# Performance work log

Measured on AMD Instinct MI355X. Metric: run time of the kernel, lower is better.

Reference implementation:

```python
import jax, jax.numpy as jnp
import numpy as np

N, E, T, D, M, G = 131072, 524288, 4, 128, 256, 4096
VOCAB, GH, L, PASSES = 100, 512, 128, 4


def setup_inputs() -> dict:
    key = jax.random.key(0)
    ks = jax.random.split(key, 20)
    node_types = jax.random.randint(ks[0], (N,), 0, VOCAB)
    edge_src = jax.random.randint(ks[1], (E,), 0, N)
    edge_dst = jax.random.randint(ks[2], (E,), 0, N)
    edge_type = jax.random.randint(ks[3], (E,), 0, T)
    inner = jnp.sort(jax.random.randint(ks[4], (G - 1,), 0, N))
    ptr = jnp.concatenate([jnp.zeros((1,), jnp.int64 if inner.dtype == jnp.int64 else jnp.int32),
                           inner, jnp.full((1,), N, inner.dtype)])
    s = 1.0 / np.sqrt(D)
    emb = jax.random.normal(ks[5], (VOCAB, D), jnp.float32)
    W_msg = jax.random.normal(ks[6], (T, M, D), jnp.float32) * s
    b_msg = jax.random.normal(ks[7], (T, M), jnp.float32) * s
    W_ih = jax.random.normal(ks[8], (3 * D, M), jnp.float32) * (1.0 / np.sqrt(M))
    W_hh = jax.random.normal(ks[9], (3 * D, D), jnp.float32) * s
    b_ih = jax.random.normal(ks[10], (3 * D,), jnp.float32) * s
    b_hh = jax.random.normal(ks[11], (3 * D,), jnp.float32) * s
    W_gate = jax.random.normal(ks[12], (1, D), jnp.float32) * s
    b_gate = jax.random.normal(ks[13], (1,), jnp.float32) * s
    W_n2g = jax.random.normal(ks[14], (GH, D), jnp.float32) * s
    b_n2g = jax.random.normal(ks[15], (GH,), jnp.float32) * s
    W_loc = jax.random.normal(ks[16], (L, GH), jnp.float32) * (1.0 / np.sqrt(GH))
    b_loc = jax.random.normal(ks[17], (L,), jnp.float32) * (1.0 / np.sqrt(GH))
    W_lv = jax.random.normal(ks[18], (L, GH), jnp.float32) * (1.0 / np.sqrt(GH))
    b_lv = jax.random.normal(ks[19], (L,), jnp.float32) * (1.0 / np.sqrt(GH))
    return dict(node_types=node_types, edge_src=edge_src, edge_dst=edge_dst,
                edge_type=edge_type, ptr=ptr, emb=emb, W_msg=W_msg, b_msg=b_msg,
                W_ih=W_ih, W_hh=W_hh, b_ih=b_ih, b_hh=b_hh, W_gate=W_gate,
                b_gate=b_gate, W_n2g=W_n2g, b_n2g=b_n2g, W_loc=W_loc, b_loc=b_loc,
                W_lv=W_lv, b_lv=b_lv)


def _ggnn_pass(h, edge_src, edge_dst, edge_type, W_msg, b_msg, W_ih, W_hh, b_ih, b_hh):
    # per-edge-type linear on all nodes: [T, N, M]
    msgs_all = jnp.einsum('nd,tmd->tnm', h, W_msg) + b_msg[:, None, :]
    # gather the message of the edge's type at its source node: [E, M]
    e_msg = msgs_all[edge_type, edge_src]
    # sparse adjacency matmul == scatter-add of source messages into destinations
    agg = jax.ops.segment_sum(e_msg, edge_dst, num_segments=h.shape[0])
    m = jax.nn.relu(agg)
    # torch GRUCell
    gi = m @ W_ih.T + b_ih      # [N, 3D]
    gh = h @ W_hh.T + b_hh      # [N, 3D]
    d = h.shape[1]
    ir, iz, inn = gi[:, :d], gi[:, d:2 * d], gi[:, 2 * d:]
    hr, hz, hn = gh[:, :d], gh[:, d:2 * d], gh[:, 2 * d:]
    r = jax.nn.sigmoid(ir + hr)
    z = jax.nn.sigmoid(iz + hz)
    n = jnp.tanh(inn + r * hn)
    return (1.0 - z) * n + z * h


def reference(node_types, edge_src, edge_dst, edge_type, ptr, emb, W_msg, b_msg,
              W_ih, W_hh, b_ih, b_hh, W_gate, b_gate, W_n2g, b_n2g,
              W_loc, b_loc, W_lv, b_lv):
    h = emb[node_types]  # [N, D]
    for _ in range(PASSES):
        h = _ggnn_pass(h, edge_src, edge_dst, edge_type,
                       W_msg, b_msg, W_ih, W_hh, b_ih, b_hh)
    # gated segment readout (equivalent to per-graph attn @ h slices)
    gate = jax.nn.sigmoid(h @ W_gate.T + b_gate)        # [N, 1]
    hg = h @ W_n2g.T + b_n2g                            # [N, GH]
    seg = jnp.searchsorted(ptr, jnp.arange(h.shape[0]), side='right') - 1
    h_graph = jax.ops.segment_sum(gate * hg, seg, num_segments=ptr.shape[0] - 1)
    z_loc = h_graph @ W_loc.T + b_loc
    z_logvar = h_graph @ W_lv.T + b_lv
    return (z_loc, z_logvar)
```

## Files before the change

kernel.cpp:

```cpp
#include <hip/hip_runtime.h>
#include <cstdint>
#include <cstddef>

#define NN 131072
#define EE 524288
#define GG 4096
#define NPASS 4

typedef __attribute__((ext_vector_type(4))) float f32x4;
typedef __attribute__((ext_vector_type(8))) short bfrag;

__device__ __forceinline__ unsigned short f2bf(float f) {
  union { float f; unsigned u; } v; v.f = f;
  unsigned r = v.u + 0x7fffu + ((v.u >> 16) & 1u);
  return (unsigned short)(r >> 16);
}
__device__ __forceinline__ float bf2f(unsigned short h) {
  union { unsigned u; float f; } v; v.u = ((unsigned)h) << 16;
  return v.f;
}
__device__ __forceinline__ unsigned pack2(float x, float y) {
  return (unsigned)f2bf(x) | ((unsigned)f2bf(y) << 16);
}
__device__ __forceinline__ float sigm(float x) { return 1.f / (1.f + __expf(-x)); }

__device__ __forceinline__ void cp16(unsigned short* l, const unsigned short* g) {
  __builtin_amdgcn_global_load_lds(
      (const __attribute__((address_space(1))) unsigned int*)g,
      (__attribute__((address_space(3))) unsigned int*)l, 16, 0, 0);
}

__global__ void prep_wb(const float* __restrict__ Wmsg, unsigned short* __restrict__ Wb) {
  int idx = blockIdx.x * 256 + threadIdx.x;
  if (idx >= 256 * 512) return;
  int m = idx >> 9, k = idx & 511;
  int t = k >> 7, d = k & 127;
  Wb[idx] = f2bf(Wmsg[((size_t)t * 256 + m) * 128 + d]);
}

__global__ void prep_wgru(const float* __restrict__ Wih, const float* __restrict__ Whh,
                          unsigned short* __restrict__ Wgru) {
  int idx = blockIdx.x * 256 + threadIdx.x;
  if (idx >= 512 * 384) return;
  int j = idx / 384, kk = idx % 384;
  float v;
  if (kk < 256) v = (j < 384) ? Wih[j * 256 + kk] : 0.f;
  else          v = (j < 256) ? Whh[j * 128 + (kk - 256)]
                   : ((j >= 384) ? Whh[(j - 128) * 128 + (kk - 256)] : 0.f);
  int g = (j < 128) ? 0 : (j < 256) ? 1 : (j < 384) ? 2 : 3;
  int d = j & 127;
  Wgru[(size_t)(4 * d + g) * 384 + kk] = f2bf(v);
}

__global__ void prep_bias(const float* __restrict__ bih, const float* __restrict__ bhh,
                          float* __restrict__ biasg) {
  int j = blockIdx.x * 256 + threadIdx.x;
  if (j >= 512) return;
  float v;
  if (j < 256) v = bih[j] + bhh[j];
  else if (j < 384) v = bih[j];
  else v = bhh[j - 128];
  int g = (j < 128) ? 0 : (j < 256) ? 1 : (j < 384) ? 2 : 3;
  int d = j & 127;
  biasg[4 * d + g] = v;
}

__global__ void compose_k(const float* __restrict__ Wloc, const float* __restrict__ Wlv,
                          const float* __restrict__ Wn2g, float* __restrict__ WcT) {
  int b = blockIdx.x;
  int jl = threadIdx.x >> 7, d = threadIdx.x & 127;
  int j = b * 2 + jl;
  const float* wx = (j < 128) ? Wloc + (size_t)j * 512 : Wlv + (size_t)(j - 128) * 512;
  float acc = 0.f;
  for (int k = 0; k < 512; k++) acc += wx[k] * Wn2g[k * 128 + d];
  WcT[d * 256 + j] = acc;
}

__global__ void cvec_k(const float* __restrict__ Wloc, const float* __restrict__ Wlv,
                       const float* __restrict__ bn2g, float* __restrict__ cvec) {
  int j = threadIdx.x;
  const float* wx = (j < 128) ? Wloc + (size_t)j * 512 : Wlv + (size_t)(j - 128) * 512;
  float a = 0.f;
  for (int k = 0; k < 512; k++) a += wx[k] * bn2g[k];
  cvec[j] = a;
}

__global__ void init_h(const int* __restrict__ nt, const float* __restrict__ emb,
                       unsigned short* __restrict__ H) {
  size_t idx = (size_t)blockIdx.x * 256 + threadIdx.x;
  int n = (int)(idx >> 7), d = (int)(idx & 127);
  H[idx] = f2bf(emb[(size_t)nt[n] * 128 + d]);
}

__global__ void cnt4_k(const int* __restrict__ edst, const int* __restrict__ etype,
                       int* __restrict__ cnti) {
  int e = blockIdx.x * 256 + threadIdx.x;
  if (e >= EE) return;
  atomicAdd(&cnti[edst[e] * 4 + etype[e]], 1);
}

__global__ void degsum_k(const int* __restrict__ cnti, int* __restrict__ deg,
                         float* __restrict__ cnt) {
  int n = blockIdx.x * 256 + threadIdx.x;
  if (n >= NN) return;
  int4 c4 = *(const int4*)&cnti[n * 4];
  deg[n] = c4.x + c4.y + c4.z + c4.w;
  float4 f4 = make_float4((float)c4.x, (float)c4.y, (float)c4.z, (float)c4.w);
  *(float4*)&cnt[n * 4] = f4;
}

__global__ __launch_bounds__(1024) void scan_k(const int* __restrict__ deg,
                                               int* __restrict__ rowptr,
                                               int* __restrict__ cursor) {
  __shared__ int part[1024];
  int t = threadIdx.x;
  int base = t * 128;
  int s = 0;
  for (int i = 0; i < 128; i++) s += deg[base + i];
  part[t] = s;
  __syncthreads();
  for (int off = 1; off < 1024; off <<= 1) {
    int v = (t >= off) ? part[t - off] : 0;
    __syncthreads();
    part[t] += v;
    __syncthreads();
  }
  int run = part[t] - s;
  for (int i = 0; i < 128; i++) {
    rowptr[base + i] = run;
    cursor[base + i] = run;
    run += deg[base + i];
  }
  if (t == 1023) rowptr[NN] = run;
}

__global__ void fill_k(const int* __restrict__ esrc, const int* __restrict__ edst,
                       const int* __restrict__ etype, int* __restrict__ cursor,
                       unsigned* __restrict__ epack) {
  int e = blockIdx.x * 256 + threadIdx.x;
  if (e >= EE) return;
  int pos = atomicAdd(&cursor[edst[e]], 1);
  epack[pos] = ((unsigned)etype[e] << 17) | (unsigned)esrc[e];
}

__global__ __launch_bounds__(256) void agg_k(const int* __restrict__ rowptr,
                                             const unsigned* __restrict__ epack,
                                             const unsigned short* __restrict__ H,
                                             unsigned short* __restrict__ s) {
  int n = blockIdx.x * 4 + (threadIdx.x >> 6);
  int lane = threadIdx.x & 63;
  int beg = rowptr[n], end = rowptr[n + 1];
  const unsigned short* hbase = H + lane * 2;
  float a0 = 0.f, a1 = 0.f, b0 = 0.f, b1 = 0.f;
  float c0 = 0.f, c1 = 0.f, d0 = 0.f, d1 = 0.f;
#define ACCUM(P, HV)                                              \
  {                                                               \
    int t_ = (int)((P) >> 17);                                    \
    float v0_ = bf2f((unsigned short)((HV) & 0xffffu));           \
    float v1_ = bf2f((unsigned short)((HV) >> 16));               \
    if (t_ == 0)      { a0 += v0_; a1 += v1_; }                   \
    else if (t_ == 1) { b0 += v0_; b1 += v1_; }                   \
    else if (t_ == 2) { c0 += v0_; c1 += v1_; }                   \
    else              { d0 += v0_; d1 += v1_; }                   \
  }
  for (int base = beg; base < end; base += 64) {
    int cnt = end - base;
    if (cnt > 64) cnt = 64;
    int mye = base + lane;
    unsigned ep = (mye < end) ? epack[mye] : 0u;
    if (cnt > 0) {
      unsigned p = (unsigned)__shfl((int)ep, 0);
      unsigned hv = *(const unsigned*)&hbase[(size_t)(p & 0x1FFFFu) * 128];
      for (int j = 1; j < cnt; j++) {
        unsigned pn = (unsigned)__shfl((int)ep, j);
        unsigned hvn = *(const unsigned*)&hbase[(size_t)(pn & 0x1FFFFu) * 128];
        ACCUM(p, hv);
        p = pn;
        hv = hvn;
      }
      ACCUM(p, hv);
    }
  }
#undef ACCUM
  unsigned short* srow = s + (size_t)n * 512;
  *(unsigned*)&srow[0 * 128 + lane * 2] = pack2(a0, a1);
  *(unsigned*)&srow[1 * 128 + lane * 2] = pack2(b0, b1);
  *(unsigned*)&srow[2 * 128 + lane * 2] = pack2(c0, c1);
  *(unsigned*)&srow[3 * 128 + lane * 2] = pack2(d0, d1);
}

__global__ __launch_bounds__(512, 4) void msgemm_k(
    unsigned short* __restrict__ s, const float* __restrict__ cnt,
    const unsigned short* __restrict__ Wb, const float* __restrict__ bmsg) {
  __shared__ __align__(16) unsigned short As[2][128 * 32];
  __shared__ __align__(16) unsigned short Bs[2][256 * 32];
  int i0 = blockIdx.x * 128;
  int tid = threadIdx.x, lane = tid & 63, w = tid >> 6;
  int wi = w >> 1, wj = w & 1;
  int q = lane >> 4, r = lane & 15;
  int srow = tid >> 2;
  int swcol = ((tid & 3) ^ ((srow >> 1) & 3)) * 8;

  const unsigned short* sP = s + (size_t)(i0 + srow) * 512 + swcol;
  const unsigned short* WbP = Wb + (size_t)srow * 512 + swcol;

  int aoff[2], boff[8];
#pragma unroll
  for (int rt = 0; rt < 2; rt++) {
    int row = wi * 32 + rt * 16 + r;
    aoff[rt] = row * 32 + (q ^ ((row >> 1) & 3)) * 8;
  }
#pragma unroll
  for (int ct = 0; ct < 8; ct++) {
    int row = wj * 128 + ct * 16 + r;
    boff[ct] = row * 32 + (q ^ ((row >> 1) & 3)) * 8;
  }

  f32x4 acc[2][8];
#pragma unroll
  for (int a = 0; a < 2; a++)
#pragma unroll
    for (int b = 0; b < 8; b++) acc[a][b] = f32x4{0.f, 0.f, 0.f, 0.f};

  cp16(&As[0][w * 512], sP);
#pragma unroll
  for (int c = 0; c < 2; c++)
    cp16(&Bs[0][c * 4096 + w * 512], WbP + (size_t)(c * 128) * 512);
  __syncthreads();

  for (int ks = 0; ks < 16; ks++) {
    int b = ks & 1;
    if (ks < 15) {
      int nb = b ^ 1;
      cp16(&As[nb][w * 512], sP + (ks + 1) * 32);
#pragma unroll
      for (int c = 0; c < 2; c++)
        cp16(&Bs[nb][c * 4096 + w * 512],
             WbP + (size_t)(c * 128) * 512 + (ks + 1) * 32);
    }
    bfrag af[2];
#pragma unroll
    for (int rt = 0; rt < 2; rt++) af[rt] = *(const bfrag*)&As[b][aoff[rt]];
#pragma unroll
    for (int ct = 0; ct < 8; ct++) {
      bfrag bfr = *(const bfrag*)&Bs[b][boff[ct]];
#pragma unroll
      for (int rt = 0; rt < 2; rt++)
        acc[rt][ct] =
            __builtin_amdgcn_mfma_f32_16x16x32_bf16(af[rt], bfr, acc[rt][ct], 0, 0, 0);
    }
    __syncthreads();
  }

#pragma unroll
  for (int ct = 0; ct < 8; ct++) {
    int j = wj * 128 + ct * 16 + r;
    float b0 = bmsg[j], b1 = bmsg[256 + j], b2 = bmsg[512 + j], b3 = bmsg[768 + j];
#pragma unroll
    for (int rt = 0; rt < 2; rt++) {
#pragma unroll
      for (int reg = 0; reg < 4; reg++) {
        int il = wi * 32 + rt * 16 + q * 4 + reg;
        float4 c4 = *(const float4*)&cnt[(size_t)(i0 + il) * 4];
        float v = acc[rt][ct][reg] + c4.x * b0 + c4.y * b1 + c4.z * b2 + c4.w * b3;
        v = v > 0.f ? v : 0.f;
        s[(size_t)(i0 + il) * 512 + j] = f2bf(v);
      }
    }
  }
}

__global__ __launch_bounds__(512, 4) void grugemm_k(
    const unsigned short* __restrict__ m,
    const unsigned short* __restrict__ Hc, unsigned short* __restrict__ Hn,
    const unsigned short* __restrict__ Wgru, const float* __restrict__ biasg) {
  __shared__ __align__(16) unsigned short As[2][128 * 32];
  __shared__ __align__(16) unsigned short Bs[2][256 * 32];
  int wg = (blockIdx.x & 7) * 256 + (blockIdx.x >> 3);
  int bcol = wg & 1;
  int i0 = (wg >> 1) * 128;
  int tid = threadIdx.x, lane = tid & 63, w = tid >> 6;
  int wi = w >> 1, wj = w & 1;
  int q = lane >> 4, r = lane & 15;
  int srow = tid >> 2;
  int swcol = ((tid & 3) ^ ((srow >> 1) & 3)) * 8;

  const unsigned short* mP = m + (size_t)(i0 + srow) * 512 + swcol;
  const unsigned short* hP = Hc + (size_t)(i0 + srow) * 128 + swcol;
  const unsigned short* WgP = Wgru + (size_t)(bcol * 256 + srow) * 384 + swcol;

  int aoff[2], boff[8];
#pragma unroll
  for (int rt = 0; rt < 2; rt++) {
    int row = wi * 32 + rt * 16 + r;
    aoff[rt] = row * 32 + (q ^ ((row >> 1) & 3)) * 8;
  }
#pragma unroll
  for (int ct = 0; ct < 8; ct++) {
    int row = wj * 128 + ct * 16 + r;
    boff[ct] = row * 32 + (q ^ ((row >> 1) & 3)) * 8;
  }

  f32x4 acc[2][8];
#pragma unroll
  for (int a = 0; a < 2; a++)
#pragma unroll
    for (int b = 0; b < 8; b++) acc[a][b] = f32x4{0.f, 0.f, 0.f, 0.f};

  cp16(&As[0][w * 512], mP);
#pragma unroll
  for (int c = 0; c < 2; c++)
    cp16(&Bs[0][c * 4096 + w * 512], WgP + (size_t)(c * 128) * 384);
  __syncthreads();

  for (int ks = 0; ks < 12; ks++) {
    int b = ks & 1;
    if (ks < 11) {
      int nb = b ^ 1;
      int nks = ks + 1;
      const unsigned short* aSrc =
          (nks < 8) ? (mP + nks * 32) : (hP + (nks - 8) * 32);
      cp16(&As[nb][w * 512], aSrc);
#pragma unroll
      for (int c = 0; c < 2; c++)
        cp16(&Bs[nb][c * 4096 + w * 512],
             WgP + (size_t)(c * 128) * 384 + nks * 32);
    }
    bfrag af[2];
#pragma unroll
    for (int rt = 0; rt < 2; rt++) af[rt] = *(const bfrag*)&As[b][aoff[rt]];
#pragma unroll
    for (int ct = 0; ct < 8; ct++) {
      bfrag bfr = *(const bfrag*)&Bs[b][boff[ct]];
#pragma unroll
      for (int rt = 0; rt < 2; rt++)
        acc[rt][ct] =
            __builtin_amdgcn_mfma_f32_16x16x32_bf16(af[rt], bfr, acc[rt][ct], 0, 0, 0);
    }
    __syncthreads();
  }

  int rr = r & 3;
  bool s1 = (lane & 1) != 0, s2 = (lane & 2) != 0;
#pragma unroll
  for (int ct = 0; ct < 8; ct++) {
    float bias = biasg[bcol * 256 + wj * 128 + ct * 16 + r];
    int d = bcol * 64 + wj * 32 + ct * 4 + (r >> 2);
#pragma unroll
    for (int rt = 0; rt < 2; rt++) {
      float v0 = acc[rt][ct][0] + bias;
      float v1 = acc[rt][ct][1] + bias;
      float v2 = acc[rt][ct][2] + bias;
      float v3 = acc[rt][ct][3] + bias;
      float t, rcv;
      t = s1 ? v0 : v1; rcv = __shfl_xor(t, 1);
      v0 = s1 ? rcv : v0; v1 = s1 ? v1 : rcv;
      t = s1 ? v2 : v3; rcv = __shfl_xor(t, 1);
      v2 = s1 ? rcv : v2; v3 = s1 ? v3 : rcv;
      t = s2 ? v0 : v2; rcv = __shfl_xor(t, 2);
      v0 = s2 ? rcv : v0; v2 = s2 ? v2 : rcv;
      t = s2 ? v1 : v3; rcv = __shfl_xor(t, 2);
      v1 = s2 ? rcv : v1; v3 = s2 ? v3 : rcv;
      int i = i0 + wi * 32 + rt * 16 + q * 4 + rr;
      size_t hoff = (size_t)i * 128 + d;
      float hold = bf2f(Hc[hoff]);
      float rg = sigm(v0), zg = sigm(v1);
      float ng = tanhf(v2 + rg * v3);
      Hn[hoff] = f2bf((1.f - zg) * ng + zg * hold);
    }
  }
}

__global__ __launch_bounds__(256) void gate_k(const unsigned short* __restrict__ H,
                                              const float* __restrict__ Wg,
                                              const float* __restrict__ bg,
                                              float* __restrict__ gate) {
  __shared__ float wg[128];
  if (threadIdx.x < 128) wg[threadIdx.x] = Wg[threadIdx.x];
  __syncthreads();
  int g = threadIdx.x >> 4, sub = threadIdx.x & 15;
  int n = blockIdx.x * 16 + g;
  const unsigned short* hr = H + (size_t)n * 128;
  float p = 0.f;
  for (int k = sub; k < 128; k += 16) p += bf2f(hr[k]) * wg[k];
  p += __shfl_xor(p, 1);
  p += __shfl_xor(p, 2);
  p += __shfl_xor(p, 4);
  p += __shfl_xor(p, 8);
  if (sub == 0) gate[n] = sigm(p + bg[0]);
}

__global__ __launch_bounds__(256) void gsum_k(const unsigned short* __restrict__ H,
                                              const float* __restrict__ gate,
                                              const int* __restrict__ ptr,
                                              float* __restrict__ gsum,
                                              float* __restrict__ sg) {
  int g = blockIdx.x * 4 + (threadIdx.x >> 6);
  int lane = threadIdx.x & 63;
  int start = ptr[g], end = ptr[g + 1];
  float a0 = 0.f, a1 = 0.f, gs = 0.f;
  for (int n = start; n < end; n++) {
    float gt = gate[n];
    unsigned hv = *(const unsigned*)&H[(size_t)n * 128 + lane * 2];
    a0 += gt * bf2f((unsigned short)(hv & 0xffffu));
    a1 += gt * bf2f((unsigned short)(hv >> 16));
    gs += gt;
  }
  gsum[(size_t)g * 128 + lane * 2] = a0;
  gsum[(size_t)g * 128 + lane * 2 + 1] = a1;
  if (lane == 0) sg[g] = gs;
}

__global__ __launch_bounds__(256) void zfinal_k(const float* __restrict__ gsum,
                                                const float* __restrict__ sg,
                                                const float* __restrict__ WcT,
                                                const float* __restrict__ cvec,
                                                const float* __restrict__ bloc,
                                                const float* __restrict__ blv,
                                                float* __restrict__ out) {
  __shared__ float gs[128];
  __shared__ float sgs;
  int g = blockIdx.x;
  int j = threadIdx.x;
  if (j < 128) gs[j] = gsum[(size_t)g * 128 + j];
  if (j == 0) sgs = sg[g];
  __syncthreads();
  float acc = (j < 128 ? bloc[j] : blv[j - 128]) + sgs * cvec[j];
  for (int d = 0; d < 128; d++) acc += gs[d] * WcT[d * 256 + j];
  size_t o = (j < 128) ? ((size_t)g * 128 + j)
                       : ((size_t)GG * 128 + (size_t)g * 128 + (j - 128));
  out[o] = acc;
}

extern "C" void kernel_launch(void* const* d_in, const int* in_sizes, int n_in,
                              void* d_out, int out_size, void* d_ws, size_t ws_size,
                              hipStream_t stream) {
  const int* node_types = (const int*)d_in[0];
  const int* esrc = (const int*)d_in[1];
  const int* edst = (const int*)d_in[2];
  const int* etype = (const int*)d_in[3];
  const int* ptr = (const int*)d_in[4];
  const float* emb = (const float*)d_in[5];
  const float* Wmsg = (const float*)d_in[6];
  const float* bmsg = (const float*)d_in[7];
  const float* Wih = (const float*)d_in[8];
  const float* Whh = (const float*)d_in[9];
  const float* bih = (const float*)d_in[10];
  const float* bhh = (const float*)d_in[11];
  const float* Wg = (const float*)d_in[12];
  const float* bg = (const float*)d_in[13];
  const float* Wn2g = (const float*)d_in[14];
  const float* bn2g = (const float*)d_in[15];
  const float* Wloc = (const float*)d_in[16];
  const float* bloc = (const float*)d_in[17];
  const float* Wlv = (const float*)d_in[18];
  const float* blv = (const float*)d_in[19];
  float* out = (float*)d_out;

  char* ws = (char*)d_ws;
  size_t off = 0;
  unsigned short* s = (unsigned short*)(ws);
  off += (size_t)NN * 512 * 2;
  unsigned short* H0 = (unsigned short*)(ws + off);
  off += (size_t)NN * 128 * 2;
  unsigned short* H1 = (unsigned short*)(ws + off);
  off += (size_t)NN * 128 * 2;
  float* cnt = (float*)(ws + off);
  off += (size_t)NN * 4 * 4;
  int* cnti = (int*)(ws + off);
  off += (size_t)NN * 4 * 4;
  int* deg = (int*)(ws + off);
  off += (size_t)NN * 4;
  int* rowptr = (int*)(ws + off);
  off += (size_t)(NN + 64) * 4;
  int* cursor = (int*)(ws + off);
  off += (size_t)NN * 4;
  unsigned* epack = (unsigned*)(ws + off);
  off += (size_t)EE * 4;
  float* gate = (float*)(ws + off);
  off += (size_t)NN * 4;
  float* gsum = (float*)(ws + off);
  off += (size_t)GG * 128 * 4;
  float* sg = (float*)(ws + off);
  off += (size_t)GG * 4;
  float* WcT = (float*)(ws + off);
  off += 128 * 256 * 4;
  float* cvec = (float*)(ws + off);
  off += 256 * 4;
  unsigned short* Wb = (unsigned short*)(ws + off);
  off += 256 * 512 * 2;
  unsigned short* Wgru = (unsigned short*)(ws + off);
  off += 512 * 384 * 2;
  float* biasg = (float*)(ws + off);
  off += 512 * 4;

  hipMemsetAsync(cnti, 0, (size_t)NN * 16, stream);
  prep_wb<<<512, 256, 0, stream>>>(Wmsg, Wb);
  prep_wgru<<<768, 256, 0, stream>>>(Wih, Whh, Wgru);
  prep_bias<<<2, 256, 0, stream>>>(bih, bhh, biasg);
  compose_k<<<128, 256, 0, stream>>>(Wloc, Wlv, Wn2g, WcT);
  cvec_k<<<1, 256, 0, stream>>>(Wloc, Wlv, bn2g, cvec);
  init_h<<<NN * 128 / 256, 256, 0, stream>>>(node_types, emb, H0);
  cnt4_k<<<EE / 256, 256, 0, stream>>>(edst, etype, cnti);
  degsum_k<<<NN / 256, 256, 0, stream>>>(cnti, deg, cnt);
  scan_k<<<1, 1024, 0, stream>>>(deg, rowptr, cursor);
  fill_k<<<EE / 256, 256, 0, stream>>>(esrc, edst, etype, cursor, epack);

  unsigned short* Hc = H0;
  unsigned short* Hn = H1;
  for (int p = 0; p < NPASS; p++) {
    agg_k<<<NN / 4, 256, 0, stream>>>(rowptr, epack, Hc, s);
    msgemm_k<<<NN / 128, 512, 0, stream>>>(s, cnt, Wb, bmsg);
    grugemm_k<<<NN / 128 * 2, 512, 0, stream>>>(s, Hc, Hn, Wgru, biasg);
    unsigned short* tmp = Hc; Hc = Hn; Hn = tmp;
  }

  gate_k<<<NN / 16, 256, 0, stream>>>(Hc, Wg, bg, gate);
  gsum_k<<<GG / 4, 256, 0, stream>>>(Hc, gate, ptr, gsum, sg);
  zfinal_k<<<GG, 256, 0, stream>>>(gsum, sg, WcT, cvec, bloc, blv, out);
}
```

Before: 1.192 ms.

## Use square 64x64 warp tiles, transpose GRU MFMA output, fast sigmoid/tanh

Both GEMM kernels change the per-wave tile from 32x128 to 64x64. Each wave now loads 4 A and 4 B fragments per k-step instead of 2 and 8, which cuts LDS fragment reads per MFMA. The GRU kernel also swaps the MFMA operands so each lane's four accumulator registers already hold the r/z/n_i/n_h gates for one element. That removes the cross-lane shuffle transpose in the epilogue. Sigmoid and tanh now use the hardware reciprocal and an exp-based tanh, which is slightly less accurate; the epilogue stores are also less coalesced, since consecutive lanes now write different nodes.

Result: slower. 1.811 ms (+51.9%).

```diff
diff --git a/kernel.cpp b/kernel.cpp
--- a/kernel.cpp
+++ b/kernel.cpp
@@ -22,7 +22,12 @@
 __device__ __forceinline__ unsigned pack2(float x, float y) {
   return (unsigned)f2bf(x) | ((unsigned)f2bf(y) << 16);
 }
-__device__ __forceinline__ float sigm(float x) { return 1.f / (1.f + __expf(-x)); }
+__device__ __forceinline__ float sigm(float x) {
+  return __builtin_amdgcn_rcpf(1.f + __expf(-x));
+}
+__device__ __forceinline__ float tanh_fast(float x) {
+  return 1.f - 2.f * __builtin_amdgcn_rcpf(1.f + __expf(2.f * x));
+}
 
 __device__ __forceinline__ void cp16(unsigned short* l, const unsigned short* g) {
   __builtin_amdgcn_global_load_lds(
@@ -196,7 +201,7 @@
   __shared__ __align__(16) unsigned short Bs[2][256 * 32];
   int i0 = blockIdx.x * 128;
   int tid = threadIdx.x, lane = tid & 63, w = tid >> 6;
-  int wi = w >> 1, wj = w & 1;
+  int wn = w & 1, wj3 = w >> 1;
   int q = lane >> 4, r = lane & 15;
   int srow = tid >> 2;
   int swcol = ((tid & 3) ^ ((srow >> 1) & 3)) * 8;
@@ -204,23 +209,23 @@
   const unsigned short* sP = s + (size_t)(i0 + srow) * 512 + swcol;
   const unsigned short* WbP = Wb + (size_t)srow * 512 + swcol;
 
-  int aoff[2], boff[8];
-#pragma unroll
-  for (int rt = 0; rt < 2; rt++) {
-    int row = wi * 32 + rt * 16 + r;
+  int aoff[4], boff[4];
+#pragma unroll
+  for (int rt = 0; rt < 4; rt++) {
+    int row = wn * 64 + rt * 16 + r;
     aoff[rt] = row * 32 + (q ^ ((row >> 1) & 3)) * 8;
   }
 #pragma unroll
-  for (int ct = 0; ct < 8; ct++) {
-    int row = wj * 128 + ct * 16 + r;
+  for (int ct = 0; ct < 4; ct++) {
+    int row = wj3 * 64 + ct * 16 + r;
     boff[ct] = row * 32 + (q ^ ((row >> 1) & 3)) * 8;
   }
 
-  f32x4 acc[2][8];
-#pragma unroll
-  for (int a = 0; a < 2; a++)
-#pragma unroll
-    for (int b = 0; b < 8; b++) acc[a][b] = f32x4{0.f, 0.f, 0.f, 0.f};
+  f32x4 acc[4][4];
+#pragma unroll
+  for (int a = 0; a < 4; a++)
+#pragma unroll
+    for (int b = 0; b < 4; b++) acc[a][b] = f32x4{0.f, 0.f, 0.f, 0.f};
 
   cp16(&As[0][w * 512], sP);
 #pragma unroll
@@ -238,14 +243,14 @@
         cp16(&Bs[nb][c * 4096 + w * 512],
              WbP + (size_t)(c * 128) * 512 + (ks + 1) * 32);
     }
-    bfrag af[2];
-#pragma unroll
-    for (int rt = 0; rt < 2; rt++) af[rt] = *(const bfrag*)&As[b][aoff[rt]];
-#pragma unroll
-    for (int ct = 0; ct < 8; ct++) {
+    bfrag af[4];
+#pragma unroll
+    for (int rt = 0; rt < 4; rt++) af[rt] = *(const bfrag*)&As[b][aoff[rt]];
+#pragma unroll
+    for (int ct = 0; ct < 4; ct++) {
       bfrag bfr = *(const bfrag*)&Bs[b][boff[ct]];
 #pragma unroll
-      for (int rt = 0; rt < 2; rt++)
+      for (int rt = 0; rt < 4; rt++)
         acc[rt][ct] =
             __builtin_amdgcn_mfma_f32_16x16x32_bf16(af[rt], bfr, acc[rt][ct], 0, 0, 0);
     }
@@ -253,14 +258,14 @@
   }
 
 #pragma unroll
-  for (int ct = 0; ct < 8; ct++) {
-    int j = wj * 128 + ct * 16 + r;
+  for (int ct = 0; ct < 4; ct++) {
+    int j = wj3 * 64 + ct * 16 + r;
     float b0 = bmsg[j], b1 = bmsg[256 + j], b2 = bmsg[512 + j], b3 = bmsg[768 + j];
 #pragma unroll
-    for (int rt = 0; rt < 2; rt++) {
+    for (int rt = 0; rt < 4; rt++) {
 #pragma unroll
       for (int reg = 0; reg < 4; reg++) {
-        int il = wi * 32 + rt * 16 + q * 4 + reg;
+        int il = wn * 64 + rt * 16 + q * 4 + reg;
         float4 c4 = *(const float4*)&cnt[(size_t)(i0 + il) * 4];
         float v = acc[rt][ct][reg] + c4.x * b0 + c4.y * b1 + c4.z * b2 + c4.w * b3;
         v = v > 0.f ? v : 0.f;
@@ -280,7 +285,7 @@
   int bcol = wg & 1;
   int i0 = (wg >> 1) * 128;
   int tid = threadIdx.x, lane = tid & 63, w = tid >> 6;
-  int wi = w >> 1, wj = w & 1;
+  int wn = w & 1, wj3 = w >> 1;
   int q = lane >> 4, r = lane & 15;
   int srow = tid >> 2;
   int swcol = ((tid & 3) ^ ((srow >> 1) & 3)) * 8;
@@ -289,23 +294,23 @@
   const unsigned short* hP = Hc + (size_t)(i0 + srow) * 128 + swcol;
   const unsigned short* WgP = Wgru + (size_t)(bcol * 256 + srow) * 384 + swcol;
 
-  int aoff[2], boff[8];
-#pragma unroll
-  for (int rt = 0; rt < 2; rt++) {
-    int row = wi * 32 + rt * 16 + r;
-    aoff[rt] = row * 32 + (q ^ ((row >> 1) & 3)) * 8;
-  }
-#pragma unroll
-  for (int ct = 0; ct < 8; ct++) {
-    int row = wj * 128 + ct * 16 + r;
-    boff[ct] = row * 32 + (q ^ ((row >> 1) & 3)) * 8;
-  }
-
-  f32x4 acc[2][8];
-#pragma unroll
-  for (int a = 0; a < 2; a++)
-#pragma unroll
-    for (int b = 0; b < 8; b++) acc[a][b] = f32x4{0.f, 0.f, 0.f, 0.f};
+  int noff[4], joff[4];
+#pragma unroll
+  for (int nt = 0; nt < 4; nt++) {
+    int row = wn * 64 + nt * 16 + r;
+    noff[nt] = row * 32 + (q ^ ((row >> 1) & 3)) * 8;
+  }
+#pragma unroll
+  for (int jt = 0; jt < 4; jt++) {
+    int row = wj3 * 64 + jt * 16 + r;
+    joff[jt] = row * 32 + (q ^ ((row >> 1) & 3)) * 8;
+  }
+
+  f32x4 acc[4][4];
+#pragma unroll
+  for (int a = 0; a < 4; a++)
+#pragma unroll
+    for (int b = 0; b < 4; b++) acc[a][b] = f32x4{0.f, 0.f, 0.f, 0.f};
 
   cp16(&As[0][w * 512], mP);
 #pragma unroll
@@ -326,46 +331,35 @@
         cp16(&Bs[nb][c * 4096 + w * 512],
              WgP + (size_t)(c * 128) * 384 + nks * 32);
     }
-    bfrag af[2];
-#pragma unroll
-    for (int rt = 0; rt < 2; rt++) af[rt] = *(const bfrag*)&As[b][aoff[rt]];
-#pragma unroll
-    for (int ct = 0; ct < 8; ct++) {
-      bfrag bfr = *(const bfrag*)&Bs[b][boff[ct]];
-#pragma unroll
-      for (int rt = 0; rt < 2; rt++)
-        acc[rt][ct] =
-            __builtin_amdgcn_mfma_f32_16x16x32_bf16(af[rt], bfr, acc[rt][ct], 0, 0, 0);
+    bfrag nf[4];
+#pragma unroll
+    for (int nt = 0; nt < 4; nt++) nf[nt] = *(const bfrag*)&As[b][noff[nt]];
+#pragma unroll
+    for (int jt = 0; jt < 4; jt++) {
+      bfrag jf = *(const bfrag*)&Bs[b][joff[jt]];
+#pragma unroll
+      for (int nt = 0; nt < 4; nt++)
+        acc[nt][jt] =
+            __builtin_amdgcn_mfma_f32_16x16x32_bf16(jf, nf[nt], acc[nt][jt], 0, 0, 0);
     }
     __syncthreads();
   }
 
-  int rr = r & 3;
-  bool s1 = (lane & 1) != 0, s2 = (lane & 2) != 0;
-#pragma unroll
-  for (int ct = 0; ct < 8; ct++) {
-    float bias = biasg[bcol * 256 + wj * 128 + ct * 16 + r];
-    int d = bcol * 64 + wj * 32 + ct * 4 + (r >> 2);
-#pragma unroll
-    for (int rt = 0; rt < 2; rt++) {
-      float v0 = acc[rt][ct][0] + bias;
-      float v1 = acc[rt][ct][1] + bias;
-      float v2 = acc[rt][ct][2] + bias;
-      float v3 = acc[rt][ct][3] + bias;
-      float t, rcv;
-      t = s1 ? v0 : v1; rcv = __shfl_xor(t, 1);
-      v0 = s1 ? rcv : v0; v1 = s1 ? v1 : rcv;
-      t = s1 ? v2 : v3; rcv = __shfl_xor(t, 1);
-      v2 = s1 ? rcv : v2; v3 = s1 ? v3 : rcv;
-      t = s2 ? v0 : v2; rcv = __shfl_xor(t, 2);
-      v0 = s2 ? rcv : v0; v2 = s2 ? v2 : rcv;
-      t = s2 ? v1 : v3; rcv = __shfl_xor(t, 2);
-      v1 = s2 ? rcv : v1; v3 = s2 ? v3 : rcv;
-      int i = i0 + wi * 32 + rt * 16 + q * 4 + rr;
-      size_t hoff = (size_t)i * 128 + d;
+#pragma unroll
+  for (int jt = 0; jt < 4; jt++) {
+    float4 b4 = *(const float4*)&biasg[bcol * 256 + wj3 * 64 + jt * 16 + 4 * q];
+    int d = bcol * 64 + wj3 * 16 + jt * 4 + q;
+#pragma unroll
+    for (int nt = 0; nt < 4; nt++) {
+      int node = i0 + wn * 64 + nt * 16 + r;
+      float v0 = acc[nt][jt][0] + b4.x;
+      float v1 = acc[nt][jt][1] + b4.y;
+      float v2 = acc[nt][jt][2] + b4.z;
+      float v3 = acc[nt][jt][3] + b4.w;
+      float rg = sigm(v0), zg = sigm(v1);
+      float ng = tanh_fast(v2 + rg * v3);
+      size_t hoff = (size_t)node * 128 + d;
       float hold = bf2f(Hc[hoff]);
-      float rg = sigm(v0), zg = sigm(v1);
-      float ng = tanhf(v2 + rg * v3);
       Hn[hoff] = f2bf((1.f - zg) * ng + zg * hold);
     }
   }
```
